# Performance work log

Hardware: AMD Instinct MI355X
Metric: run time of the kernel (lower is better)

The kernel has to match this reference:

```python
import jax, jax.numpy as jnp
import numpy as np

B, S, DIN, DOUT = 4, 2048, 4096, 4096

def setup_inputs() -> dict:
    key = jax.random.key(0)
    k1, k2, k3 = jax.random.split(key, 3)
    x = jax.random.normal(k1, (B, S, DIN), dtype=jnp.float32)
    # kaiming-uniform-like scale for weight, uniform bias in [-1/sqrt(fan_in), 1/sqrt(fan_in)]
    bound_w = 1.0 / np.sqrt(DIN)
    weight = jax.random.uniform(k2, (DOUT, DIN), minval=-bound_w, maxval=bound_w, dtype=jnp.float32)
    bias = jax.random.uniform(k3, (DOUT,), minval=-bound_w, maxval=bound_w, dtype=jnp.float32)
    kk = jnp.asarray(1.0, dtype=jnp.float32)
    aa = jnp.asarray(1.0, dtype=jnp.float32)
    return {"x": x, "weight": weight, "bias": bias, "kk": kk, "aa": aa}

def reference(x, weight, bias, kk, aa):
    # Adiabatic binarization: soft-binarize weight with w_b = aa * tanh(kk * w),
    # then standard linear y = x @ w_b.T + bias. As kk -> inf, w_b -> aa*sign(w).
    w_b = aa * jnp.tanh(kk * weight)          # [DOUT, DIN]
    y = jnp.einsum('bsi,oi->bso', x, w_b)     # [B, S, DOUT]
    return y + bias
```

## Files before the change

kernel.cpp:

```cpp
#include <hip/hip_runtime.h>
#include <stdint.h>

#define B_DIM 4
#define S_DIM 2048
#define DIN   4096
#define DOUT  4096
#define M_TOT (B_DIM * S_DIM)

typedef __attribute__((ext_vector_type(8))) short  bf16x8;
typedef __attribute__((ext_vector_type(4))) float  f32x4;
typedef __attribute__((ext_vector_type(4))) unsigned short u16x4;
typedef __attribute__((ext_vector_type(4))) float  float4v;

__device__ __forceinline__ unsigned short f2b(float f) {
  union { float f; unsigned int i; } v; v.f = f;
  unsigned int r = v.i + 0x7FFFu + ((v.i >> 16) & 1u);
  return (unsigned short)(r >> 16);
}

__global__ void cvt_fused_kernel(const float4v* __restrict__ w, u16x4* __restrict__ wbo,
                                 const float4v* __restrict__ x, u16x4* __restrict__ xbo,
                                 const float* __restrict__ kk,
                                 const float* __restrict__ aa) {
  const int bid = blockIdx.x;
  if (bid < 2048) {
    const float k = kk[0];
    const float a = aa[0];
    const int n4 = DOUT * DIN / 4;
    for (int i = bid * 256 + threadIdx.x; i < n4; i += 2048 * 256) {
      float4v v = w[i];
      u16x4 o;
#pragma unroll
      for (int j = 0; j < 4; ++j) o[j] = f2b(a * tanhf(k * v[j]));
      wbo[i] = o;
    }
  } else {
    const int n4 = M_TOT * DIN / 4;
    for (int i = (bid - 2048) * 256 + threadIdx.x; i < n4; i += 4096 * 256) {
      float4v v = x[i];
      u16x4 o;
#pragma unroll
      for (int j = 0; j < 4; ++j) o[j] = f2b(v[j]);
      xbo[i] = o;
    }
  }
}

#define BM 256
#define BN 256
#define BK 64
#define NT (DIN / BK)

__device__ __forceinline__ void glds16(const unsigned short* g, unsigned short* l) {
  __builtin_amdgcn_global_load_lds(
      (const __attribute__((address_space(1))) void*)g,
      (__attribute__((address_space(3))) void*)l,
      16, 0, 0);
}

#define BARX()    __builtin_amdgcn_s_barrier()
#define LGKM0()   asm volatile("s_waitcnt lgkmcnt(0)" ::: "memory")
#define WAITVM8() asm volatile("s_waitcnt vmcnt(8)" ::: "memory")
#define WAITVM0() asm volatile("s_waitcnt vmcnt(0)" ::: "memory")

#define RDB(dst, BLK, BUFB)                                                   \
  dst[0] = *(const bf16x8*)(bRd + (BUFB) + 0 * 2048 + (BLK));                 \
  dst[1] = *(const bf16x8*)(bRd + (BUFB) + 1 * 2048 + (BLK));                 \
  dst[2] = *(const bf16x8*)(bRd + (BUFB) + 2 * 2048 + (BLK));                 \
  dst[3] = *(const bf16x8*)(bRd + (BUFB) + 3 * 2048 + (BLK));

#define RDA4(dst, MB, BLK, BUFB)                                              \
  dst[0] = *(const bf16x8*)(aRd + (BUFB) + ((MB) + 0) * 2048 + (BLK));        \
  dst[1] = *(const bf16x8*)(aRd + (BUFB) + ((MB) + 1) * 2048 + (BLK));        \
  dst[2] = *(const bf16x8*)(aRd + (BUFB) + ((MB) + 2) * 2048 + (BLK));        \
  dst[3] = *(const bf16x8*)(aRd + (BUFB) + ((MB) + 3) * 2048 + (BLK));

#define MFMA_PH(AF, BF, MB)                                                   \
  __builtin_amdgcn_s_setprio(1);                                              \
  {                                                                           \
    _Pragma("unroll")                                                         \
    for (int i = 0; i < 4; ++i)                                               \
      _Pragma("unroll")                                                       \
      for (int ni = 0; ni < 4; ++ni)                                          \
        acc[(MB) + i][ni] = __builtin_amdgcn_mfma_f32_16x16x32_bf16(          \
            AF[i], BF[ni], acc[(MB) + i][ni], 0, 0, 0);                       \
  }                                                                           \
  __builtin_amdgcn_s_setprio(0);

#define KTILE(t, BUFB)                                                        \
  {                                                                           \
                                         \
    RDB(bfr0, blk0, BUFB);                                                    \
    RDA4(afA, 0, blk0, BUFB);                                                 \
    BARX(); LGKM0();                                                          \
    MFMA_PH(afA, bfr0, 0);                                                    \
    BARX();                                                                   \
           \
    RDA4(afB, 4, blk0, BUFB);                                                 \
    RDB(bfr1, blk1, BUFB);                                                    \
    BARX(); LGKM0();                                                          \
    MFMA_PH(afB, bfr0, 4);                                                    \
    BARX();                                                                   \
    \
    RDA4(afA, 0, blk1, BUFB);                                                 \
    RDA4(afB, 4, blk1, BUFB);                                                 \
    stageB((t) + 2);                                                          \
    BARX(); LGKM0();                                                          \
    MFMA_PH(afA, bfr1, 0);                                                    \
    BARX();                                                                   \
                          \
    stageA((t) + 2);                                                          \
    BARX();                                                                   \
    MFMA_PH(afB, bfr1, 4);                                                    \
    if ((t) + 2 < NT) { WAITVM8(); } else { WAITVM0(); }                      \
    BARX();                                                                   \
  }

__global__ __launch_bounds__(512, 2)
void gemm256_kernel(const unsigned short* __restrict__ A,
                    const unsigned short* __restrict__ Bw,
                    const float* __restrict__ bias,
                    float* __restrict__ C) {
  __shared__ unsigned short lds[2][2][BM * BK];

  const int tid  = threadIdx.x;
  const int wv   = tid >> 6;
  const int lane = tid & 63;
  const int l15  = lane & 15;
  const int quad = lane >> 4;
  const int l7   = lane & 7;
  const int rlan = lane >> 3;

  const int xcd = blockIdx.x & 7;
  const int idx = blockIdx.x >> 3;
  const int bm  = ((((xcd & 3) << 3) | (idx & 7)) << 8);
  const int bn  = ((((xcd >> 2) << 3) | (idx >> 3)) << 8);

  const unsigned short* aLane = A  + (size_t)(bm + wv * 16 + rlan) * DIN + ((l7 ^ rlan) << 3);
  const unsigned short* bLane = Bw + (size_t)(bn + wv * 16 + rlan) * DIN + ((l7 ^ rlan) << 3);

  auto stageA = [&](int kt) {
    if (kt >= NT) return;
    const int buf = kt & 1;
    const size_t ko = (size_t)kt * BK;
#pragma unroll
    for (int hr = 0; hr < 2; ++hr) {
      const unsigned short* ga = aLane + (size_t)hr * (128 * DIN) + ko;
      unsigned short* la = &lds[buf][0][hr * (128 * BK) + wv * (16 * BK)];
      glds16(ga, la);
      glds16(ga + 8 * DIN, la + 8 * BK);
    }
  };
  auto stageB = [&](int kt) {
    if (kt >= NT) return;
    const int buf = kt & 1;
    const size_t ko = (size_t)kt * BK;
#pragma unroll
    for (int hr = 0; hr < 2; ++hr) {
      const unsigned short* gb = bLane + (size_t)hr * (128 * DIN) + ko;
      unsigned short* lb = &lds[buf][1][hr * (128 * BK) + wv * (16 * BK)];
      glds16(gb, lb);
      glds16(gb + 8 * DIN, lb + 8 * BK);
    }
  };

  stageB(0); stageA(0); stageB(1); stageA(1);

  const int hA   = wv >> 2;
  const int hB   = (wv & 3) >> 1;
  const int wloc = wv & 1;
  const char* aRd = (const char*)&lds[0][0][0] + hA * 16384 + l15 * 128;
  const char* bRd = (const char*)&lds[0][1][0] + hB * 16384 + wloc * 8192 + l15 * 128;
  const int blk0 = ((0 + quad) ^ l7) * 16;
  const int blk1 = ((4 + quad) ^ l7) * 16;

  f32x4  acc[8][4] = {};
  bf16x8 bfr0[4], bfr1[4], afA[4], afB[4];

  WAITVM8();
  BARX();

#pragma unroll 1
  for (int t = 0; t < NT; t += 2) {
    KTILE(t, 0);
    KTILE(t + 1, 65536);
  }

  const int wm = (wv >> 2) * 128;
  const int wn = (wv & 3) * 64;
#pragma unroll
  for (int ni = 0; ni < 4; ++ni) {
    const int col = bn + wn + ni * 16 + l15;
    const float bv = bias[col];
#pragma unroll
    for (int mi = 0; mi < 8; ++mi) {
      const int row0 = bm + wm + mi * 16 + quad * 4;
#pragma unroll
      for (int e = 0; e < 4; ++e)
        C[(size_t)(row0 + e) * DOUT + col] = acc[mi][ni][e] + bv;
    }
  }
}

extern "C" void kernel_launch(void* const* d_in, const int* in_sizes, int n_in,
                              void* d_out, int out_size, void* d_ws, size_t ws_size,
                              hipStream_t stream) {
  const float* x    = (const float*)d_in[0];
  const float* w    = (const float*)d_in[1];
  const float* bias = (const float*)d_in[2];
  const float* kk   = (const float*)d_in[3];
  const float* aa   = (const float*)d_in[4];
  float* out = (float*)d_out;

  unsigned short* wb = (unsigned short*)d_ws;
  unsigned short* xb = wb + (size_t)DOUT * DIN;

  cvt_fused_kernel<<<6144, 256, 0, stream>>>(
      (const float4v*)w, (u16x4*)wb, (const float4v*)x, (u16x4*)xb, kk, aa);

  gemm256_kernel<<<dim3(512), dim3(512), 0, stream>>>(xb, wb, bias, out);
}
```

Before: 519.8 us.

## Interleave half-tile A/B global-to-LDS loads across MFMA phases, drop a barrier

```diff
diff --git a/kernel.cpp b/kernel.cpp
--- a/kernel.cpp
+++ b/kernel.cpp
@@ -60,7 +60,7 @@
 
 #define BARX()    __builtin_amdgcn_s_barrier()
 #define LGKM0()   asm volatile("s_waitcnt lgkmcnt(0)" ::: "memory")
-#define WAITVM8() asm volatile("s_waitcnt vmcnt(8)" ::: "memory")
+#define WAITVM4() asm volatile("s_waitcnt vmcnt(4)" ::: "memory")
 #define WAITVM0() asm volatile("s_waitcnt vmcnt(0)" ::: "memory")
 
 #define RDB(dst, BLK, BUFB)                                                   \
@@ -89,30 +89,31 @@
 
 #define KTILE(t, BUFB)                                                        \
   {                                                                           \
-                                         \
+                         \
     RDB(bfr0, blk0, BUFB);                                                    \
     RDA4(afA, 0, blk0, BUFB);                                                 \
+    stageAh((t) + 1, 0);                                                      \
     BARX(); LGKM0();                                                          \
     MFMA_PH(afA, bfr0, 0);                                                    \
     BARX();                                                                   \
            \
     RDA4(afB, 4, blk0, BUFB);                                                 \
     RDB(bfr1, blk1, BUFB);                                                    \
+    stageAh((t) + 1, 1);                                                      \
     BARX(); LGKM0();                                                          \
     MFMA_PH(afB, bfr0, 4);                                                    \
     BARX();                                                                   \
-    \
+                       \
     RDA4(afA, 0, blk1, BUFB);                                                 \
     RDA4(afB, 4, blk1, BUFB);                                                 \
-    stageB((t) + 2);                                                          \
+    stageBh((t) + 2, 0);                                                      \
     BARX(); LGKM0();                                                          \
     MFMA_PH(afA, bfr1, 0);                                                    \
     BARX();                                                                   \
-                          \
-    stageA((t) + 2);                                                          \
-    BARX();                                                                   \
+                   \
+    stageBh((t) + 2, 1);                                                      \
     MFMA_PH(afB, bfr1, 4);                                                    \
-    if ((t) + 2 < NT) { WAITVM8(); } else { WAITVM0(); }                      \
+    if ((t) + 2 < NT) { WAITVM4(); } else { WAITVM0(); }                      \
     BARX();                                                                   \
   }
 
@@ -139,32 +140,23 @@
   const unsigned short* aLane = A  + (size_t)(bm + wv * 16 + rlan) * DIN + ((l7 ^ rlan) << 3);
   const unsigned short* bLane = Bw + (size_t)(bn + wv * 16 + rlan) * DIN + ((l7 ^ rlan) << 3);
 
-  auto stageA = [&](int kt) {
+  auto stageAh = [&](int kt, int hr) {
     if (kt >= NT) return;
-    const int buf = kt & 1;
-    const size_t ko = (size_t)kt * BK;
-#pragma unroll
-    for (int hr = 0; hr < 2; ++hr) {
-      const unsigned short* ga = aLane + (size_t)hr * (128 * DIN) + ko;
-      unsigned short* la = &lds[buf][0][hr * (128 * BK) + wv * (16 * BK)];
-      glds16(ga, la);
-      glds16(ga + 8 * DIN, la + 8 * BK);
-    }
+    const unsigned short* ga = aLane + (size_t)hr * (128 * DIN) + (size_t)kt * BK;
+    unsigned short* la = &lds[kt & 1][0][hr * (128 * BK) + wv * (16 * BK)];
+    glds16(ga, la);
+    glds16(ga + 8 * DIN, la + 8 * BK);
   };
-  auto stageB = [&](int kt) {
+  auto stageBh = [&](int kt, int hr) {
     if (kt >= NT) return;
-    const int buf = kt & 1;
-    const size_t ko = (size_t)kt * BK;
-#pragma unroll
-    for (int hr = 0; hr < 2; ++hr) {
-      const unsigned short* gb = bLane + (size_t)hr * (128 * DIN) + ko;
-      unsigned short* lb = &lds[buf][1][hr * (128 * BK) + wv * (16 * BK)];
-      glds16(gb, lb);
-      glds16(gb + 8 * DIN, lb + 8 * BK);
-    }
+    const unsigned short* gb = bLane + (size_t)hr * (128 * DIN) + (size_t)kt * BK;
+    unsigned short* lb = &lds[kt & 1][1][hr * (128 * BK) + wv * (16 * BK)];
+    glds16(gb, lb);
+    glds16(gb + 8 * DIN, lb + 8 * BK);
   };
 
-  stageB(0); stageA(0); stageB(1); stageA(1);
+  stageBh(0, 0); stageBh(0, 1); stageAh(0, 0); stageAh(0, 1);
+  stageBh(1, 0); stageBh(1, 1);
 
   const int hA   = wv >> 2;
   const int hB   = (wv & 3) >> 1;
@@ -177,7 +169,7 @@
   f32x4  acc[8][4] = {};
   bf16x8 bfr0[4], bfr1[4], afA[4], afB[4];
 
-  WAITVM8();
+  WAITVM4();
   BARX();
 
 #pragma unroll 1
```

Result: faster. 493.9 us (-5.0%).
